# Kernel tuning notes

Measured on AMD Instinct MI355X. Metric: run time of the kernel, lower is better.

The kernel has to match this reference:

```python
import jax, jax.numpy as jnp
import numpy as np

L, K, HID, OUT, B, N, E = 2, 3, 64, 32, 8, 10000, 160000


def setup_inputs() -> dict:
    key = jax.random.key(0)
    ks = jax.random.split(key, 12)
    s = 0.05
    return {
        "edge_weight": jax.random.uniform(ks[1], (E,), dtype=jnp.float32),
        "hidden_states": jax.random.normal(ks[2], (L, B, N, HID), dtype=jnp.float32),
        "go_input": jax.random.normal(ks[3], (B, N, HID), dtype=jnp.float32),
        "Wz": jax.random.normal(ks[4], (L, 2, K, 2 * HID, HID), dtype=jnp.float32) * s,
        "bz": jnp.zeros((L, HID), dtype=jnp.float32),
        "Wr": jax.random.normal(ks[5], (L, 2, K, 2 * HID, HID), dtype=jnp.float32) * s,
        "br": jnp.zeros((L, HID), dtype=jnp.float32),
        "Wh": jax.random.normal(ks[6], (L, 2, K, 2 * HID, HID), dtype=jnp.float32) * s,
        "bh": jnp.zeros((L, HID), dtype=jnp.float32),
        "proj_W": jax.random.normal(ks[7], (HID, OUT), dtype=jnp.float32) * s,
        "proj_b": jnp.zeros((OUT,), dtype=jnp.float32),
        "edge_index": jax.random.randint(ks[0], (2, E), 0, N, dtype=jnp.int32),
    }


def _prop(z, s_idx, d_idx, nw):
    # z: [B,N,F]; aggregate nw-weighted source features at destinations
    m = z[:, s_idx, :] * nw[None, :, None]  # [B,E,F]
    return jnp.zeros_like(z).at[:, d_idx, :].add(m)


def _dconv(x, W, b, src, dst, norm_out, norm_in):
    # x: [B,N,Fin]; W: [2,K,Fin,Fout] (dir 0 = forward walk, dir 1 = reverse)
    H = jnp.einsum('bnf,fo->bno', x, W[0, 0] + W[1, 0])  # T0 shared
    To_pp, Ti_pp = x, x
    To_p = _prop(x, src, dst, norm_out)
    Ti_p = _prop(x, dst, src, norm_in)
    H = H + jnp.einsum('bnf,fo->bno', To_p, W[0, 1]) + jnp.einsum('bnf,fo->bno', Ti_p, W[1, 1])
    for k in range(2, K):  # Chebyshev recursion over hops
        To = 2.0 * _prop(To_p, src, dst, norm_out) - To_pp
        Ti = 2.0 * _prop(Ti_p, dst, src, norm_in) - Ti_pp
        H = H + jnp.einsum('bnf,fo->bno', To, W[0, k]) + jnp.einsum('bnf,fo->bno', Ti, W[1, k])
        To_pp, To_p = To_p, To
        Ti_pp, Ti_p = Ti_p, Ti
    return H + b


def _cell(x, h, Wz, bz, Wr, br, Wh, bh, src, dst, no, ni):
    xh = jnp.concatenate([x, h], axis=-1)
    Z = jax.nn.sigmoid(_dconv(xh, Wz, bz, src, dst, no, ni))
    R = jax.nn.sigmoid(_dconv(xh, Wr, br, src, dst, no, ni))
    Ht = jnp.tanh(_dconv(jnp.concatenate([x, R * h], axis=-1), Wh, bh, src, dst, no, ni))
    return Z * h + (1.0 - Z) * Ht


def reference(edge_weight, hidden_states, go_input, Wz, bz, Wr, br, Wh, bh, proj_W, proj_b, edge_index):
    src, dst = edge_index[0], edge_index[1]
    deg_out = jax.ops.segment_sum(edge_weight, src, num_segments=N)
    deg_in = jax.ops.segment_sum(edge_weight, dst, num_segments=N)
    inv_out = 1.0 / jnp.where(deg_out > 0, deg_out, 1.0)
    inv_in = 1.0 / jnp.where(deg_in > 0, deg_in, 1.0)
    norm_out = edge_weight * inv_out[src]
    norm_in = edge_weight * inv_in[dst]

    cur = go_input
    last = cur
    for l in range(L):  # small fixed layer loop (dropout=0 -> identity)
        last = _cell(cur, hidden_states[l], Wz[l], bz[l], Wr[l], br[l], Wh[l], bh[l],
                     src, dst, norm_out, norm_in)
        if l < L - 1:
            cur = last
    return jnp.einsum('bnh,ho->bno', last, proj_W) + proj_b
```

## Files before the change

kernel.cpp:

```cpp
#include <hip/hip_runtime.h>
#include <math.h>

#define NL 2
#define KK 3
#define HIDD 64
#define OUTD 32
#define NB 8
#define NN 10000
#define NE 160000
#define ROWS 80000
#define WSTRIDE (128*HIDD)

typedef __attribute__((ext_vector_type(8))) short bf16x8;
typedef __attribute__((ext_vector_type(8))) unsigned short u16x8;
typedef __attribute__((ext_vector_type(4))) unsigned short u16x4;
typedef __attribute__((ext_vector_type(4))) float f32x4;

__device__ __forceinline__ ushort f2b(float x) {
    union { float f; unsigned u; } v; v.f = x;
    unsigned r = (v.u + 0x7fff + ((v.u >> 16) & 1)) >> 16;
    return (ushort)r;
}
__device__ __forceinline__ float b2f(ushort u) {
    union { unsigned u; float f; } v; v.u = (unsigned)u << 16;
    return v.f;
}

__global__ void zero_kernel(int* p, long n) {
    long t = (long)blockIdx.x * blockDim.x + threadIdx.x;
    if (t < n) p[t] = 0;
}

__global__ void deg_cnt_kernel(const float* __restrict__ w, const int* __restrict__ src,
                               const int* __restrict__ dst, float* deg_out, float* deg_in,
                               int* cnt_f, int* cnt_r) {
    int e = blockIdx.x * blockDim.x + threadIdx.x;
    if (e >= NE) return;
    int s = src[e], d = dst[e];
    float we = w[e];
    atomicAdd(&deg_out[s], we);
    atomicAdd(&deg_in[d], we);
    atomicAdd(&cnt_f[d], 1);
    atomicAdd(&cnt_r[s], 1);
}

__global__ void scan_kernel(const int* __restrict__ cnt, int* __restrict__ off) {
    __shared__ int part[256];
    const int CH = (NN + 255) / 256;
    int t = threadIdx.x;
    int s = 0;
    for (int i = 0; i < CH; ++i) {
        int idx = t * CH + i;
        if (idx < NN) s += cnt[idx];
    }
    part[t] = s;
    __syncthreads();
    if (t == 0) {
        int run = 0;
        for (int i = 0; i < 256; ++i) { int v = part[i]; part[i] = run; run += v; }
        off[NN] = run;
    }
    __syncthreads();
    int run = part[t];
    for (int i = 0; i < CH; ++i) {
        int idx = t * CH + i;
        if (idx < NN) { off[idx] = run; run += cnt[idx]; }
    }
}

__global__ void copy_pos_kernel(const int* __restrict__ off_f, const int* __restrict__ off_r,
                                int* pos_f, int* pos_r) {
    int t = blockIdx.x * blockDim.x + threadIdx.x;
    if (t < NN) { pos_f[t] = off_f[t]; pos_r[t] = off_r[t]; }
}

__global__ void fill_kernel(const float* __restrict__ w, const int* __restrict__ src,
                            const int* __restrict__ dst, const float* __restrict__ deg_out,
                            const float* __restrict__ deg_in,
                            int* pos_f, int* pos_r,
                            int* col_f, float* w_f, int* col_r, float* w_r) {
    int e = blockIdx.x * blockDim.x + threadIdx.x;
    if (e >= NE) return;
    int s = src[e], d = dst[e];
    float we = w[e];
    float dgo = deg_out[s]; dgo = (dgo > 0.f) ? dgo : 1.f;
    float dgi = deg_in[d];  dgi = (dgi > 0.f) ? dgi : 1.f;
    int pf = atomicAdd(&pos_f[d], 1);
    col_f[pf] = s; w_f[pf] = we / dgo;
    int pr = atomicAdd(&pos_r[s], 1);
    col_r[pr] = d; w_r[pr] = we / dgi;
}

__global__ void convW_kernel(const float* __restrict__ Wz, const float* __restrict__ Wr,
                             const float* __restrict__ Wh, ushort* __restrict__ Wt) {
    int t = blockIdx.x * 256 + threadIdx.x;
    if (t >= 2 * 3 * 2 * 3 * 64 * 128) return;
    int f = t & 127;
    int r1 = t >> 7;
    int o = r1 & 63;
    int r2 = r1 >> 6;
    int k = r2 % 3;
    int r3 = r2 / 3;
    int d = r3 & 1;
    int r4 = r3 >> 1;
    int g = r4 % 3;
    int l = r4 / 3;
    const float* W = (g == 0) ? Wz : (g == 1) ? Wr : Wh;
    auto idx = [&](int dd_, int kk_) {
        return (((long)(l * 2 + dd_) * 3 + kk_) * 128 + f) * 64 + o;
    };
    float v = W[idx(d, k)];
    if (k == 0 && d == 0)
        v += W[idx(1, 0)] - W[idx(0, 2)] - W[idx(1, 2)];
    if (k == 2) v *= 2.f;
    Wt[t] = f2b(v);
}

__global__ void convX_perm(const float* __restrict__ in, ushort* __restrict__ xh, int c,
                           float* __restrict__ hp) {
    long t = (long)blockIdx.x * blockDim.x + threadIdx.x;
    if (t >= (long)ROWS * 16) return;
    int q = (int)(t & 15);
    long rowin = t >> 4;
    int b = (int)(rowin / NN);
    int n = (int)(rowin - (long)b * NN);
    f32x4 v = __builtin_nontemporal_load((const f32x4*)&in[t * 4]);
    u16x4 r;
    r.x = f2b(v.x); r.y = f2b(v.y); r.z = f2b(v.z); r.w = f2b(v.w);
    long orow = (long)n * 8 + b;
    *(u16x4*)&xh[orow * 128 + c * 64 + q * 4] = r;
    if (hp) *(f32x4*)&hp[orow * 64 + q * 4] = v;
}

struct PropCfg {
    const ushort* X[2];
    const int*    off[2];
    const int*    col[2];
    const float*  w[2];
    ushort*       out[2];
};

template<int HALF, int NDIR>
__global__ __launch_bounds__(128) void prop_slice(PropCfg C) {
    constexpr int LPG = HALF ? 16 : 32;
    constexpr int FL  = HALF ? 8 : 16;
    constexpr int GPB = 128 / LPG;
    int bid = blockIdx.x;
    int b = bid & 7;
    int r = bid >> 3;
    int dir, tile;
    if (NDIR == 2) { dir = r & 1; tile = r >> 1; }
    else           { dir = 0;     tile = r; }
    int g    = threadIdx.x / LPG;
    int lil  = threadIdx.x % LPG;
    int fl   = lil % FL;
    int eh   = lil / FL;
    int n = tile * GPB + g;
    const ushort* X   = C.X[dir];
    const int*    off = C.off[dir];
    const int*    col = C.col[dir];
    const float*  w   = C.w[dir];
    ushort*       out = C.out[dir];
    int s = off[n], e = off[n + 1];
    int eo = b * 128 + (HALF ? 64 : 0) + fl * 8;
    float acc[8];
    #pragma unroll
    for (int i = 0; i < 8; ++i) acc[i] = 0.f;
    int j = s + 2 * eh;
    for (; j + 2 <= e; j += 4) {
        int c0 = col[j], c1 = col[j + 1];
        float w0 = w[j], w1 = w[j + 1];
        u16x8 v0 = *(const u16x8*)&X[(long)c0 * 1024 + eo];
        u16x8 v1 = *(const u16x8*)&X[(long)c1 * 1024 + eo];
        #pragma unroll
        for (int i = 0; i < 8; ++i) acc[i] = fmaf(b2f(v0[i]), w0, acc[i]);
        #pragma unroll
        for (int i = 0; i < 8; ++i) acc[i] = fmaf(b2f(v1[i]), w1, acc[i]);
    }
    if (j < e) {
        u16x8 v = *(const u16x8*)&X[(long)col[j] * 1024 + eo];
        float ww = w[j];
        #pragma unroll
        for (int i = 0; i < 8; ++i) acc[i] = fmaf(b2f(v[i]), ww, acc[i]);
        if (j + 1 < e) {
            u16x8 v1 = *(const u16x8*)&X[(long)col[j + 1] * 1024 + eo];
            float w1 = w[j + 1];
            #pragma unroll
            for (int i = 0; i < 8; ++i) acc[i] = fmaf(b2f(v1[i]), w1, acc[i]);
        }
    }
    #pragma unroll
    for (int i = 0; i < 8; ++i) acc[i] += __shfl_xor(acc[i], FL);
    if (eh == 0) {
        long o = (long)n * 1024 + eo;
        u16x8 rr;
        #pragma unroll
        for (int i = 0; i < 8; ++i) rr[i] = f2b(acc[i]);
        *(u16x8*)&out[o] = rr;
    }
}

struct GM5 {
    const ushort* Xb[5];
    const ushort* Wa[10];
    const ushort* Wb[10];
};

template<int DUAL>
__global__ __launch_bounds__(512, 4) void mfma_lds(GM5 A,
        const float* __restrict__ bias0, const float* __restrict__ bias1,
        const float* __restrict__ hp, float* __restrict__ Z,
        ushort* __restrict__ xh, const float* __restrict__ Zg,
        float* __restrict__ outF, int writeF) {
    constexpr int MI = DUAL ? 2 : 1;
    __shared__ ushort sx[2][16384];
    int tid  = threadIdx.x;
    int lane = tid & 63;
    int wid  = tid >> 6;
    int lr = lane & 15;
    int lk = lane >> 4;
    int gate  = DUAL ? (wid >> 2) : 0;
    int wrow0 = DUAL ? ((wid & 3) * 32) : (wid * 16);

    f32x4 acc[MI][4];
    #pragma unroll
    for (int i = 0; i < MI; ++i)
        #pragma unroll
        for (int j = 0; j < 4; ++j)
            acc[i][j] = (f32x4){0.f, 0.f, 0.f, 0.f};

    u16x8 streg[4];
    auto load_tile = [&](int t) {
        const u16x8* g = (const u16x8*)(A.Xb[t] + (size_t)blockIdx.x * 16384);
        #pragma unroll
        for (int k = 0; k < 4; ++k) streg[k] = g[tid + k * 512];
    };
    auto write_tile = [&](int bi) {
        #pragma unroll
        for (int k = 0; k < 4; ++k) {
            int unit = tid + k * 512;
            int row = unit >> 4, c16 = unit & 15;
            int u2 = (row << 4) | (c16 ^ (row & 7));
            *(u16x8*)&sx[bi][u2 << 3] = streg[k];
        }
    };

    load_tile(0);
    write_tile(0);
    __syncthreads();

    int cur = 0;
    #pragma unroll
    for (int t = 0; t < 5; ++t) {
        if (t < 4) load_tile(t + 1);
        #pragma unroll
        for (int c = 0; c < 2; ++c) {
            const ushort* Wp = DUAL ? (gate ? A.Wb[c * 5 + t] : A.Wa[c * 5 + t])
                                    : A.Wa[c * 5 + t];
            bf16x8 b[2][4];
            #pragma unroll
            for (int ks = 0; ks < 2; ++ks)
                #pragma unroll
                for (int ni = 0; ni < 4; ++ni)
                    b[ks][ni] = *(const bf16x8*)&Wp[(ni * 16 + lr) * 128 +
                                                    ks * 32 + lk * 8];
            #pragma unroll
            for (int ks = 0; ks < 2; ++ks)
                #pragma unroll
                for (int mi = 0; mi < MI; ++mi) {
                    int r = wrow0 + mi * 16 + lr;
                    int c16 = (c << 3) | (ks << 2) | lk;
                    bf16x8 av = *(const bf16x8*)&sx[cur][(r << 7) +
                                                         ((c16 ^ (r & 7)) << 3)];
                    #pragma unroll
                    for (int ni = 0; ni < 4; ++ni)
                        acc[mi][ni] = __builtin_amdgcn_mfma_f32_16x16x32_bf16(
                            av, b[ks][ni], acc[mi][ni], 0, 0, 0);
                }
        }
        if (t < 4) {
            write_tile(cur ^ 1);
            __syncthreads();
            cur ^= 1;
        }
    }

    if (DUAL) {
        const float* bias = gate ? bias1 : bias0;
        #pragma unroll
        for (int mi = 0; mi < MI; ++mi) {
            #pragma unroll
            for (int q = 0; q < 4; ++q) {
                long row = (long)blockIdx.x * 128 + wrow0 + mi * 16 + lk * 4 + q;
                #pragma unroll
                for (int ni = 0; ni < 4; ++ni) {
                    int colc = ni * 16 + lr;
                    float v = acc[mi][ni][q] + bias[colc];
                    float sg = 1.f / (1.f + expf(-v));
                    if (gate == 0) {
                        Z[row * 64 + colc] = sg;
                    } else {
                        float hv = hp[row * 64 + colc];
                        xh[row * 128 + 64 + colc] = f2b(sg * hv);
                    }
                }
            }
        }
    } else {
        #pragma unroll
        for (int mi = 0; mi < MI; ++mi) {
            #pragma unroll
            for (int q = 0; q < 4; ++q) {
                long row = (long)blockIdx.x * 128 + wrow0 + mi * 16 + lk * 4 + q;
                #pragma unroll
                for (int ni = 0; ni < 4; ++ni) {
                    int colc = ni * 16 + lr;
                    float v = acc[mi][ni][q] + bias0[colc];
                    float ht = tanhf(v);
                    float z = Zg[row * 64 + colc];
                    float hv = hp[row * 64 + colc];
                    float res = z * hv + (1.f - z) * ht;
                    if (writeF) outF[row * 64 + colc] = res;
                    else        xh[row * 128 + colc] = f2b(res);
                }
            }
        }
    }
}

__global__ void proj_kernel(const float* __restrict__ last, const float* __restrict__ W,
                            const float* __restrict__ bias, float* __restrict__ out) {
    long t = (long)blockIdx.x * blockDim.x + threadIdx.x;
    if (t >= (long)ROWS * OUTD) return;
    long row = t >> 5;
    int  o   = (int)(t & 31);
    int n = (int)(row >> 3), b = (int)(row & 7);
    float acc = bias[o];
    #pragma unroll
    for (int hh = 0; hh < HIDD; ++hh)
        acc = fmaf(last[row * 64 + hh], W[hh * OUTD + o], acc);
    out[((long)b * NN + n) * 32 + o] = acc;
}

extern "C" void kernel_launch(void* const* d_in, const int* in_sizes, int n_in,
                              void* d_out, int out_size, void* d_ws, size_t ws_size,
                              hipStream_t stream) {
    const float* edge_weight = (const float*)d_in[0];
    const float* hidden      = (const float*)d_in[1];
    const float* go_input    = (const float*)d_in[2];
    const float* Wz = (const float*)d_in[3];
    const float* bz = (const float*)d_in[4];
    const float* Wr = (const float*)d_in[5];
    const float* br = (const float*)d_in[6];
    const float* Wh = (const float*)d_in[7];
    const float* bh = (const float*)d_in[8];
    const float* projW = (const float*)d_in[9];
    const float* projb = (const float*)d_in[10];
    const int*   eidx  = (const int*)d_in[11];
    const int* src = eidx;
    const int* dst = eidx + NE;
    float* out = (float*)d_out;

    char* p = (char*)d_ws;
    auto alloc = [&](size_t bytes) { char* r = p; p += (bytes + 15) & ~(size_t)15; return r; };
    float* deg_out = (float*)alloc(NN * 4);
    float* deg_in  = (float*)alloc(NN * 4);
    int*   cnt_f   = (int*)alloc(NN * 4);
    int*   cnt_r   = (int*)alloc(NN * 4);
    int*   off_f   = (int*)alloc((NN + 4) * 4);
    int*   off_r   = (int*)alloc((NN + 4) * 4);
    int*   pos_f   = (int*)alloc(NN * 4);
    int*   pos_r   = (int*)alloc(NN * 4);
    int*   col_f   = (int*)alloc(NE * 4);
    float* w_f     = (float*)alloc(NE * 4);
    int*   col_r   = (int*)alloc(NE * 4);
    float* w_r     = (float*)alloc(NE * 4);
    ushort* Wt     = (ushort*)alloc((size_t)2 * 3 * 2 * 3 * 64 * 128 * 2);
    const size_t XB = (size_t)ROWS * 128 * 2;
    ushort* xh  = (ushort*)alloc(XB);
    ushort* Tf1 = (ushort*)alloc(XB);
    ushort* Tf2 = (ushort*)alloc(XB);
    ushort* Tr1 = (ushort*)alloc(XB);
    ushort* Tr2 = (ushort*)alloc(XB);
    float*  Zbuf = (float*)alloc((size_t)ROWS * HIDD * 4);
    float*  hp   = (float*)alloc((size_t)ROWS * HIDD * 4);
    if ((size_t)(p - (char*)d_ws) > ws_size) return;

    const int TB = 256;
    const int EGRID = (NE + TB - 1) / TB;
    const int NGRID = (NN + TB - 1) / TB;

    zero_kernel<<<(4 * NN + TB - 1) / TB, TB, 0, stream>>>((int*)deg_out, 4 * NN);
    deg_cnt_kernel<<<EGRID, TB, 0, stream>>>(edge_weight, src, dst, deg_out, deg_in, cnt_f, cnt_r);
    scan_kernel<<<1, 256, 0, stream>>>(cnt_f, off_f);
    scan_kernel<<<1, 256, 0, stream>>>(cnt_r, off_r);
    copy_pos_kernel<<<NGRID, TB, 0, stream>>>(off_f, off_r, pos_f, pos_r);
    fill_kernel<<<EGRID, TB, 0, stream>>>(edge_weight, src, dst, deg_out, deg_in,
                                          pos_f, pos_r, col_f, w_f, col_r, w_r);

    convW_kernel<<<2304, 256, 0, stream>>>(Wz, Wr, Wh, Wt);
    convX_perm<<<5000, 256, 0, stream>>>(go_input, xh, 0, nullptr);

    auto wt_term = [&](int l, int g, int d, int k, int c) -> const ushort* {
        return Wt + ((((long)((l * 3 + g) * 2 + d) * 3 + k) * 64) * 128) + (long)c * 64;
    };
    const int dd[5]  = {0, 0, 0, 1, 1};
    const int kk2[5] = {0, 1, 2, 1, 2};

    for (int l = 0; l < NL; ++l) {
        const float* h = hidden + (long)l * ROWS * HIDD;
        convX_perm<<<5000, 256, 0, stream>>>(h, xh, 1, hp);

        {
            PropCfg c1{};
            c1.X[0] = xh;  c1.off[0] = off_f; c1.col[0] = col_f; c1.w[0] = w_f; c1.out[0] = Tf1;
            c1.X[1] = xh;  c1.off[1] = off_r; c1.col[1] = col_r; c1.w[1] = w_r; c1.out[1] = Tr1;
            prop_slice<0, 2><<<(NN / 4) * 2 * 8, 128, 0, stream>>>(c1);
            PropCfg c2f{};
            c2f.X[0] = Tf1;
            c2f.off[0] = off_f; c2f.col[0] = col_f; c2f.w[0] = w_f; c2f.out[0] = Tf2;
            prop_slice<0, 1><<<(NN / 4) * 8, 128, 0, stream>>>(c2f);
            PropCfg c2r{};
            c2r.X[0] = Tr1;
            c2r.off[0] = off_r; c2r.col[0] = col_r; c2r.w[0] = w_r; c2r.out[0] = Tr2;
            prop_slice<0, 1><<<(NN / 4) * 8, 128, 0, stream>>>(c2r);
        }

        const ushort* xs[5] = {xh, Tf1, Tf2, Tr1, Tr2};
        GM5 A{};
        for (int i = 0; i < 5; ++i) {
            A.Xb[i] = xs[i];
            A.Wa[i]     = wt_term(l, 0, dd[i], kk2[i], 0);
            A.Wa[5 + i] = wt_term(l, 0, dd[i], kk2[i], 1);
            A.Wb[i]     = wt_term(l, 1, dd[i], kk2[i], 0);
            A.Wb[5 + i] = wt_term(l, 1, dd[i], kk2[i], 1);
        }
        mfma_lds<1><<<ROWS / 128, 512, 0, stream>>>(A, bz + l * HIDD, br + l * HIDD,
                                                    hp, Zbuf, xh, nullptr, nullptr, 0);

        {
            PropCfg c1{};
            c1.X[0] = xh;  c1.off[0] = off_f; c1.col[0] = col_f; c1.w[0] = w_f; c1.out[0] = Tf1;
            c1.X[1] = xh;  c1.off[1] = off_r; c1.col[1] = col_r; c1.w[1] = w_r; c1.out[1] = Tr1;
            prop_slice<1, 2><<<(NN / 8) * 2 * 8, 128, 0, stream>>>(c1);
            PropCfg c2{};
            c2.X[0] = Tf1;
            c2.off[0] = off_f; c2.col[0] = col_f; c2.w[0] = w_f; c2.out[0] = Tf2;
            c2.X[1] = Tr1;
            c2.off[1] = off_r; c2.col[1] = col_r; c2.w[1] = w_r; c2.out[1] = Tr2;
            prop_slice<1, 2><<<(NN / 8) * 2 * 8, 128, 0, stream>>>(c2);
        }

        GM5 Ah{};
        for (int i = 0; i < 5; ++i) {
            Ah.Xb[i] = xs[i];
            Ah.Wa[i]     = wt_term(l, 2, dd[i], kk2[i], 0);
            Ah.Wa[5 + i] = wt_term(l, 2, dd[i], kk2[i], 1);
        }
        mfma_lds<0><<<ROWS / 128, 512, 0, stream>>>(Ah, bh + l * HIDD, nullptr,
                                                    hp, nullptr, xh, Zbuf, Zbuf,
                                                    (l == NL - 1) ? 1 : 0);
    }

    proj_kernel<<<(int)(((long)ROWS * OUTD + TB - 1) / TB), TB, 0, stream>>>(
        Zbuf, projW, projb, out);
}
```

Measured before the change: 933.2 us.

## Prefetch all five input tiles up front and merge second-hop propagation launches

The MFMA kernel now issues global loads for all five input tiles into registers at the start, then writes and computes them in sequence through double-buffered LDS. This takes global memory latency off the per-tile critical path, at the cost of many more live registers, so the launch bounds drop from 4 to 2 blocks per SM and occupancy falls. Separately, the two single-direction second-hop propagation launches in the first gate stage are merged into one dual-direction launch, which removes a launch and lets both directions run concurrently.

```diff
diff --git a/kernel.cpp b/kernel.cpp
--- a/kernel.cpp
+++ b/kernel.cpp
@@ -206,8 +206,53 @@
     const ushort* Wb[10];
 };
 
+#define LOADT(st, t)                                                               \
+    {                                                                              \
+        const u16x8* gg = (const u16x8*)(A.Xb[t] + (size_t)blockIdx.x * 16384);    \
+        _Pragma("unroll")                                                          \
+        for (int k = 0; k < 4; ++k) st[k] = gg[tid + k * 512];                     \
+    }
+
+#define WRITET(st, bi)                                                             \
+    {                                                                              \
+        _Pragma("unroll")                                                          \
+        for (int k = 0; k < 4; ++k) {                                              \
+            int unit = tid + k * 512;                                              \
+            int row = unit >> 4, c16 = unit & 15;                                  \
+            int u2 = (row << 4) | (c16 ^ (row & 7));                               \
+            *(u16x8*)&sx[bi][u2 << 3] = st[k];                                     \
+        }                                                                          \
+    }
+
+#define COMPUTET(t, bi)                                                            \
+    _Pragma("unroll")                                                              \
+    for (int c = 0; c < 2; ++c) {                                                  \
+        const ushort* Wp = DUAL ? (gate ? A.Wb[c * 5 + t] : A.Wa[c * 5 + t])       \
+                                : A.Wa[c * 5 + t];                                 \
+        bf16x8 bfr[2][4];                                                          \
+        _Pragma("unroll")                                                          \
+        for (int ks = 0; ks < 2; ++ks)                                             \
+            _Pragma("unroll")                                                      \
+            for (int ni = 0; ni < 4; ++ni)                                         \
+                bfr[ks][ni] = *(const bf16x8*)&Wp[(ni * 16 + lr) * 128 +           \
+                                                  ks * 32 + lk * 8];               \
+        _Pragma("unroll")                                                          \
+        for (int ks = 0; ks < 2; ++ks)                                             \
+            _Pragma("unroll")                                                      \
+            for (int mi = 0; mi < MI; ++mi) {                                      \
+                int rr_ = wrow0 + mi * 16 + lr;                                    \
+                int c16 = (c << 3) | (ks << 2) | lk;                               \
+                bf16x8 av = *(const bf16x8*)&sx[bi][(rr_ << 7) +                   \
+                                                    ((c16 ^ (rr_ & 7)) << 3)];     \
+                _Pragma("unroll")                                                  \
+                for (int ni = 0; ni < 4; ++ni)                                     \
+                    acc[mi][ni] = __builtin_amdgcn_mfma_f32_16x16x32_bf16(         \
+                        av, bfr[ks][ni], acc[mi][ni], 0, 0, 0);                    \
+            }                                                                      \
+    }
+
 template<int DUAL>
-__global__ __launch_bounds__(512, 4) void mfma_lds(GM5 A,
+__global__ __launch_bounds__(512, 2) void mfma_lds(GM5 A,
         const float* __restrict__ bias0, const float* __restrict__ bias1,
         const float* __restrict__ hp, float* __restrict__ Z,
         ushort* __restrict__ xh, const float* __restrict__ Zg,
@@ -229,61 +274,19 @@
         for (int j = 0; j < 4; ++j)
             acc[i][j] = (f32x4){0.f, 0.f, 0.f, 0.f};
 
-    u16x8 streg[4];
-    auto load_tile = [&](int t) {
-        const u16x8* g = (const u16x8*)(A.Xb[t] + (size_t)blockIdx.x * 16384);
-        #pragma unroll
-        for (int k = 0; k < 4; ++k) streg[k] = g[tid + k * 512];
-    };
-    auto write_tile = [&](int bi) {
-        #pragma unroll
-        for (int k = 0; k < 4; ++k) {
-            int unit = tid + k * 512;
-            int row = unit >> 4, c16 = unit & 15;
-            int u2 = (row << 4) | (c16 ^ (row & 7));
-            *(u16x8*)&sx[bi][u2 << 3] = streg[k];
-        }
-    };
-
-    load_tile(0);
-    write_tile(0);
-    __syncthreads();
-
-    int cur = 0;
-    #pragma unroll
-    for (int t = 0; t < 5; ++t) {
-        if (t < 4) load_tile(t + 1);
-        #pragma unroll
-        for (int c = 0; c < 2; ++c) {
-            const ushort* Wp = DUAL ? (gate ? A.Wb[c * 5 + t] : A.Wa[c * 5 + t])
-                                    : A.Wa[c * 5 + t];
-            bf16x8 b[2][4];
-            #pragma unroll
-            for (int ks = 0; ks < 2; ++ks)
-                #pragma unroll
-                for (int ni = 0; ni < 4; ++ni)
-                    b[ks][ni] = *(const bf16x8*)&Wp[(ni * 16 + lr) * 128 +
-                                                    ks * 32 + lk * 8];
-            #pragma unroll
-            for (int ks = 0; ks < 2; ++ks)
-                #pragma unroll
-                for (int mi = 0; mi < MI; ++mi) {
-                    int r = wrow0 + mi * 16 + lr;
-                    int c16 = (c << 3) | (ks << 2) | lk;
-                    bf16x8 av = *(const bf16x8*)&sx[cur][(r << 7) +
-                                                         ((c16 ^ (r & 7)) << 3)];
-                    #pragma unroll
-                    for (int ni = 0; ni < 4; ++ni)
-                        acc[mi][ni] = __builtin_amdgcn_mfma_f32_16x16x32_bf16(
-                            av, b[ks][ni], acc[mi][ni], 0, 0, 0);
-                }
-        }
-        if (t < 4) {
-            write_tile(cur ^ 1);
-            __syncthreads();
-            cur ^= 1;
-        }
-    }
+    u16x8 st0[4], st1[4], st2[4], st3[4], st4[4];
+    LOADT(st0, 0); LOADT(st1, 1); LOADT(st2, 2); LOADT(st3, 3); LOADT(st4, 4);
+
+    WRITET(st0, 0); __syncthreads();
+    COMPUTET(0, 0);
+    WRITET(st1, 1); __syncthreads();
+    COMPUTET(1, 1);
+    WRITET(st2, 0); __syncthreads();
+    COMPUTET(2, 0);
+    WRITET(st3, 1); __syncthreads();
+    COMPUTET(3, 1);
+    WRITET(st4, 0); __syncthreads();
+    COMPUTET(4, 0);
 
     if (DUAL) {
         const float* bias = gate ? bias1 : bias0;
@@ -416,14 +419,10 @@
             c1.X[0] = xh;  c1.off[0] = off_f; c1.col[0] = col_f; c1.w[0] = w_f; c1.out[0] = Tf1;
             c1.X[1] = xh;  c1.off[1] = off_r; c1.col[1] = col_r; c1.w[1] = w_r; c1.out[1] = Tr1;
             prop_slice<0, 2><<<(NN / 4) * 2 * 8, 128, 0, stream>>>(c1);
-            PropCfg c2f{};
-            c2f.X[0] = Tf1;
-            c2f.off[0] = off_f; c2f.col[0] = col_f; c2f.w[0] = w_f; c2f.out[0] = Tf2;
-            prop_slice<0, 1><<<(NN / 4) * 8, 128, 0, stream>>>(c2f);
-            PropCfg c2r{};
-            c2r.X[0] = Tr1;
-            c2r.off[0] = off_r; c2r.col[0] = col_r; c2r.w[0] = w_r; c2r.out[0] = Tr2;
-            prop_slice<0, 1><<<(NN / 4) * 8, 128, 0, stream>>>(c2r);
+            PropCfg c2{};
+            c2.X[0] = Tf1; c2.off[0] = off_f; c2.col[0] = col_f; c2.w[0] = w_f; c2.out[0] = Tf2;
+            c2.X[1] = Tr1; c2.off[1] = off_r; c2.col[1] = col_r; c2.w[1] = w_r; c2.out[1] = Tr2;
+            prop_slice<0, 2><<<(NN / 4) * 2 * 8, 128, 0, stream>>>(c2);
         }
 
         const ushort* xs[5] = {xh, Tf1, Tf2, Tr1, Tr2};
@@ -444,10 +443,8 @@
             c1.X[1] = xh;  c1.off[1] = off_r; c1.col[1] = col_r; c1.w[1] = w_r; c1.out[1] = Tr1;
             prop_slice<1, 2><<<(NN / 8) * 2 * 8, 128, 0, stream>>>(c1);
             PropCfg c2{};
-            c2.X[0] = Tf1;
-            c2.off[0] = off_f; c2.col[0] = col_f; c2.w[0] = w_f; c2.out[0] = Tf2;
-            c2.X[1] = Tr1;
-            c2.off[1] = off_r; c2.col[1] = col_r; c2.w[1] = w_r; c2.out[1] = Tr2;
+            c2.X[0] = Tf1; c2.off[0] = off_f; c2.col[0] = col_f; c2.w[0] = w_f; c2.out[0] = Tf2;
+            c2.X[1] = Tr1; c2.off[1] = off_r; c2.col[1] = col_r; c2.w[1] = w_r; c2.out[1] = Tr2;
             prop_slice<1, 2><<<(NN / 8) * 2 * 8, 128, 0, stream>>>(c2);
         }
 
```

New measurement: 993.8 us. +6.5%, slower.
